# Performance work log

Hardware: AMD Instinct MI355X
Metric: run time of the kernel (lower is better)

The kernel has to match this reference:

```python
import jax, jax.numpy as jnp
import numpy as np

EPS = 1e-5  # torch LayerNorm default


def _ln(x, g, b):
    m = jnp.mean(x, axis=-1, keepdims=True)
    v = jnp.mean((x - m) ** 2, axis=-1, keepdims=True)
    return (x - m) / jnp.sqrt(v + EPS) * g + b


def setup_inputs() -> dict:
    key = jax.random.key(0)
    ks = jax.random.split(key, 16)
    B, C, H, S, FF, BINS = 2048, 20, 256, 64, 512, 128
    f32 = jnp.float32
    def w(k, shape, s=0.02):
        return jax.random.normal(k, shape, f32) * s
    return {
        "bitplanes": jax.random.normal(ks[0], (B, C, 8, 8), f32),
        "conv1_w": w(ks[1], (H, C, 3, 3), 0.05), "conv1_b": jnp.zeros((H,), f32),
        "conv2_w": w(ks[2], (H, H, 3, 3), 0.05), "conv2_b": jnp.zeros((H,), f32),
        "in_proj_w": w(ks[3], (3 * H, H)), "in_proj_b": jnp.zeros((3 * H,), f32),
        "out_proj_w": w(ks[4], (H, H)), "out_proj_b": jnp.zeros((H,), f32),
        "ln1_g": jnp.ones((H,), f32), "ln1_b": jnp.zeros((H,), f32),
        "ff1_w": w(ks[5], (FF, H)), "ff1_b": jnp.zeros((FF,), f32),
        "ff2_w": w(ks[6], (H, FF)), "ff2_b": jnp.zeros((H,), f32),
        "ln2_g": jnp.ones((H,), f32), "ln2_b": jnp.zeros((H,), f32),
        "be1_w": w(ks[7], (H, H * S)), "be1_b": jnp.zeros((H,), f32),
        "be2_w": w(ks[8], (H, H)), "be2_b": jnp.zeros((H,), f32),
        "L1_w": w(ks[9], (H, 3 * H)), "L1_b": jnp.zeros((H,), f32),
        "L2_w": w(ks[10], (H, H)), "L2_b": jnp.zeros((H,), f32),
        "Lln_g": jnp.ones((H,), f32), "Lln_b": jnp.zeros((H,), f32),
        "H1_w": w(ks[11], (H, 2 * H)), "H1_b": jnp.zeros((H,), f32),
        "H2_w": w(ks[12], (H, H)), "H2_b": jnp.zeros((H,), f32),
        "Hln_g": jnp.ones((H,), f32), "Hln_b": jnp.zeros((H,), f32),
        "v1_w": w(ks[13], (H, H)), "v1_b": jnp.zeros((H,), f32),
        "v2_w": w(ks[14], (BINS, H)), "v2_b": jnp.zeros((BINS,), f32),
    }


def reference(bitplanes, conv1_w, conv1_b, conv2_w, conv2_b,
              in_proj_w, in_proj_b, out_proj_w, out_proj_b,
              ln1_g, ln1_b, ff1_w, ff1_b, ff2_w, ff2_b, ln2_g, ln2_b,
              be1_w, be1_b, be2_w, be2_b,
              L1_w, L1_b, L2_w, L2_b, Lln_g, Lln_b,
              H1_w, H1_b, H2_w, H2_b, Hln_g, Hln_b,
              v1_w, v1_b, v2_w, v2_b):
    N, T, Hd, nh = 8, 8, 256, 4
    B = bitplanes.shape[0]
    dn = ('NCHW', 'OIHW', 'NCHW')
    # conv encoder on 8x8 board
    x = jax.nn.relu(jax.lax.conv_general_dilated(bitplanes, conv1_w, (1, 1), 'SAME', dimension_numbers=dn) + conv1_b[None, :, None, None])
    x = jax.nn.relu(jax.lax.conv_general_dilated(x, conv2_w, (1, 1), 'SAME', dimension_numbers=dn) + conv2_b[None, :, None, None])
    x = x.reshape(B, Hd, 64).transpose(0, 2, 1)  # [B, 64, 256]
    # TransformerEncoderLayer (post-norm, eval mode => dropout off)
    qkv = x @ in_proj_w.T + in_proj_b  # [B, 64, 768]
    q, k, v = jnp.split(qkv, 3, axis=-1)
    dh = Hd // nh
    heads = lambda t: t.reshape(B, 64, nh, dh).transpose(0, 2, 1, 3)
    q, k, v = heads(q), heads(k), heads(v)
    scale = 1.0 / float(dh) ** 0.5
    a = jax.nn.softmax(jnp.einsum('bhqd,bhkd->bhqk', q, k) * scale, axis=-1)
    o = jnp.einsum('bhqk,bhkd->bhqd', a, v).transpose(0, 2, 1, 3).reshape(B, 64, Hd)
    o = o @ out_proj_w.T + out_proj_b
    x = _ln(x + o, ln1_g, ln1_b)
    ff = jax.nn.relu(x @ ff1_w.T + ff1_b) @ ff2_w.T + ff2_b
    x = _ln(x + ff, ln2_g, ln2_b)
    xf = x.reshape(B, 64 * Hd)  # [B, 16384]
    be = jax.nn.relu(jax.nn.relu(xf @ be1_w.T + be1_b) @ be2_w.T + be2_b)

    def Lnet(zL, zH):
        h = jax.nn.relu(jnp.concatenate([zL, zH, be], axis=-1) @ L1_w.T + L1_b)
        return _ln(jax.nn.relu(h @ L2_w.T + L2_b), Lln_g, Lln_b)

    def Hnet(zH, zL):
        h = jax.nn.relu(jnp.concatenate([zH, zL], axis=-1) @ H1_w.T + H1_b)
        return _ln(jax.nn.relu(h @ H2_w.T + H2_b), Hln_g, Hln_b)

    z0 = jnp.zeros((B, Hd), x.dtype)

    def step(carry, i):
        zH, zL = carry
        zL = Lnet(zL, zH)
        zH = jnp.where((i + 1) % T == 0, Hnet(zH, zL), zH)  # H update every T steps
        return (zH, zL), None

    (zH, zL), _ = jax.lax.scan(step, (z0, z0), jnp.arange(N * T - 1))
    zL = Lnet(zL, zH)
    zH = Hnet(zH, zL)
    return jax.nn.relu(zH @ v1_w.T + v1_b) @ v2_w.T + v2_b  # [B, 128]
```

## Files before the change

kernel.cpp:

```cpp
#include <hip/hip_runtime.h>
#include <hip/hip_bf16.h>
#include <math.h>

#define DEV __device__ __forceinline__

typedef __attribute__((ext_vector_type(8))) short s16x8;
typedef __attribute__((ext_vector_type(4))) float f32x4;

DEV f32x4 MF(s16x8 a, s16x8 b, f32x4 c) {
    return __builtin_amdgcn_mfma_f32_16x16x32_bf16(a, b, c, 0, 0, 0);
}

DEV void split3(float x, unsigned short& h, unsigned short& m, unsigned short& l) {
    const unsigned u = __float_as_uint(x);
    h = (unsigned short)(u >> 16);
    const float r1 = x - __uint_as_float(u & 0xffff0000u);
    const unsigned u1 = __float_as_uint(r1);
    m = (unsigned short)(u1 >> 16);
    const float r2 = r1 - __uint_as_float(u1 & 0xffff0000u);
    l = (unsigned short)(__float_as_uint(r2) >> 16);
}

DEV void split8store(const float v[8], unsigned short* d) {
    s16x8 vh, vm, vl;
#pragma unroll
    for (int j = 0; j < 8; ++j) {
        unsigned short h, m, l;
        split3(v[j], h, m, l);
        vh[j] = (short)h; vm[j] = (short)m; vl[j] = (short)l;
    }
    *(s16x8*)(d) = vh;
    *(s16x8*)(d + 512) = vm;
    *(s16x8*)(d + 1024) = vl;
}

__global__ void k_tpose(const float* __restrict__ in, float* __restrict__ out, int N, int K) {
    int total = N * K;
    for (int idx = blockIdx.x * blockDim.x + threadIdx.x; idx < total; idx += gridDim.x * blockDim.x) {
        int n = idx / K, k = idx - n * K;
        out[k * N + n] = in[idx];
    }
}

__global__ void k_wpack3(const float* __restrict__ W, unsigned short* __restrict__ WP,
                         int K, int NT, int ldw, int stride, int off) {
    const int idx = blockIdx.x * 256 + threadIdx.x;
    const int total = (K >> 5) * NT * 64;
    if (idx >= total) return;
    const int lane = idx & 63;
    const int nt = (idx >> 6) % NT;
    const int ks = idx / (64 * NT);
    const int col = nt * 16 + (lane & 15);
    const int k0 = ks * 32 + ((lane >> 4) << 3);
    const float* src = W + (size_t)col * ldw + (size_t)k0 * stride + off;
    float v[8];
#pragma unroll
    for (int j = 0; j < 8; ++j) v[j] = src[j * stride];
    split8store(v, WP + (size_t)((ks * NT + nt) * 3) * 512 + lane * 8);
}

__global__ __launch_bounds__(256) void k_conv1(const float* __restrict__ in, const float* __restrict__ w,
                                               const float* __restrict__ bias, float* __restrict__ out) {
    __shared__ __align__(16) float img[20 * 100];
    __shared__ __align__(16) float stg[16 * 260];
    const int b = blockIdx.x;
    const int t = threadIdx.x;
    for (int idx = t; idx < 2000; idx += 256) {
        int c = idx / 100, pp = idx - c * 100;
        int y = pp / 10, x = pp - y * 10;
        float v = 0.f;
        if (y >= 1 && y <= 8 && x >= 1 && x <= 8)
            v = in[((size_t)b * 20 + c) * 64 + (y - 1) * 8 + (x - 1)];
        img[idx] = v;
    }
    __syncthreads();
    const int oc = t;
    float acc[64];
    const float bz = bias[oc];
#pragma unroll
    for (int p = 0; p < 64; ++p) acc[p] = bz;
    const float* wrow = w + oc * 180;
    for (int c = 0; c < 20; ++c) {
#pragma unroll
        for (int k = 0; k < 9; ++k) {
            const int ky = k / 3, kx = k - ky * 3;
            const float wv = wrow[c * 9 + k];
            const int base = c * 100 + ky * 10 + kx;
#pragma unroll
            for (int p = 0; p < 64; ++p)
                acc[p] = fmaf(wv, img[base + p + ((p >> 3) << 1)], acc[p]);
        }
    }
#pragma unroll
    for (int cc = 0; cc < 4; ++cc) {
        __syncthreads();
#pragma unroll
        for (int p = 0; p < 16; ++p) stg[p * 260 + t] = acc[cc * 16 + p];
        __syncthreads();
        for (int idx = t; idx < 4096; idx += 256) {
            const int r = idx >> 8, c = idx & 255;
            out[((size_t)b * 64 + cc * 16 + r) * 256 + c] = fmaxf(stg[r * 260 + c], 0.f);
        }
    }
}

__global__ __launch_bounds__(256) void k_conv2mf(const float* __restrict__ a1,
                                                 const unsigned short* __restrict__ WPC2,
                                                 const float* __restrict__ bias,
                                                 float* __restrict__ xout,
                                                 unsigned short* __restrict__ xh,
                                                 unsigned short* __restrict__ xm,
                                                 unsigned short* __restrict__ xl) {
    __shared__ __align__(16) unsigned short AhS[100 * 132];
    __shared__ __align__(16) unsigned short AmS[100 * 132];
    __shared__ __align__(16) unsigned short AlS[100 * 132];
    const int b = blockIdx.x, t = threadIdx.x;
    const int wv = t >> 6, lane = t & 63;
    f32x4 acc[16];
#pragma unroll
    for (int nt = 0; nt < 16; ++nt) acc[nt] = (f32x4){0.f, 0.f, 0.f, 0.f};
    const int pl = lane & 15;
    const int py = pl >> 3, px = pl & 7;
    const int akoff = (lane >> 4) << 3;
    for (int h = 0; h < 2; ++h) {
        __syncthreads();
        for (int idx = t; idx < 12800; idx += 256) {
            const int pr = idx >> 7, c = idx & 127;
            const int Y = pr / 10, X = pr - Y * 10;
            float v = 0.f;
            if (Y >= 1 && Y <= 8 && X >= 1 && X <= 8)
                v = a1[((size_t)b * 64 + (Y - 1) * 8 + X - 1) * 256 + h * 128 + c];
            unsigned short hh, mm, ll;
            split3(v, hh, mm, ll);
            AhS[pr * 132 + c] = hh;
            AmS[pr * 132 + c] = mm;
            AlS[pr * 132 + c] = ll;
        }
        __syncthreads();
#pragma unroll
        for (int tap = 0; tap < 9; ++tap) {
            const int dy = tap / 3, dx = tap - dy * 3;
            const int prow = (wv * 2 + py + dy) * 10 + px + dx;
            const unsigned short* arh = AhS + prow * 132 + akoff;
            const unsigned short* arm = AmS + prow * 132 + akoff;
            const unsigned short* arl = AlS + prow * 132 + akoff;
#pragma unroll
            for (int ks = 0; ks < 4; ++ks) {
                const s16x8 ah = *(const s16x8*)(arh + ks * 32);
                const s16x8 am = *(const s16x8*)(arm + ks * 32);
                const s16x8 al = *(const s16x8*)(arl + ks * 32);
                const unsigned short* bp = WPC2 + (size_t)(tap * 128 + (h * 4 + ks) * 16) * 1536 + lane * 8;
#pragma unroll
                for (int nt = 0; nt < 16; ++nt) {
                    const unsigned short* bb = bp + nt * 1536;
                    const s16x8 bh = *(const s16x8*)(bb);
                    const s16x8 bm = *(const s16x8*)(bb + 512);
                    const s16x8 bl = *(const s16x8*)(bb + 1024);
                    acc[nt] = MF(ah, bh, acc[nt]);
                    acc[nt] = MF(ah, bm, acc[nt]);
                    acc[nt] = MF(am, bh, acc[nt]);
                    acc[nt] = MF(ah, bl, acc[nt]);
                    acc[nt] = MF(al, bh, acc[nt]);
                    acc[nt] = MF(am, bm, acc[nt]);
                }
            }
        }
    }
    const int prow0 = wv * 16 + ((lane >> 4) << 2);
    const int ccol = lane & 15;
#pragma unroll
    for (int nt = 0; nt < 16; ++nt) {
        const float bz = bias[nt * 16 + ccol];
#pragma unroll
        for (int i = 0; i < 4; ++i) {
            const float v = fmaxf(acc[nt][i] + bz, 0.f);
            const size_t o = ((size_t)b * 64 + prow0 + i) * 256 + nt * 16 + ccol;
            xout[o] = v;
            unsigned short hh, mm, ll;
            split3(v, hh, mm, ll);
            xh[o] = hh;
            xm[o] = mm;
            xl[o] = ll;
        }
    }
}

__global__ __launch_bounds__(512) void k_attn2(const float* __restrict__ qkv,
                                               unsigned short* __restrict__ oh, unsigned short* __restrict__ om,
                                               unsigned short* __restrict__ ol) {
    __shared__ __align__(16) float qs[64 * 65];
    __shared__ __align__(16) float ks[64 * 68];
    __shared__ __align__(16) float vs[64 * 68];
    __shared__ float pmax[8 * 64];
    __shared__ float psum[8 * 64];
    const int b = blockIdx.x, h = blockIdx.y;
    const int t = threadIdx.x;
    for (int idx = t; idx < 1024; idx += 512) {
        const int rr = idx >> 4, cc = (idx & 15) * 4;
        const float* src = qkv + ((size_t)b * 64 + rr) * 768 + h * 64 + cc;
        const float4 q4 = *(const float4*)(src);
        const float4 k4 = *(const float4*)(src + 256);
        const float4 v4 = *(const float4*)(src + 512);
        qs[rr * 65 + cc + 0] = q4.x; qs[rr * 65 + cc + 1] = q4.y;
        qs[rr * 65 + cc + 2] = q4.z; qs[rr * 65 + cc + 3] = q4.w;
        *(float4*)(ks + rr * 68 + cc) = k4;
        *(float4*)(vs + rr * 68 + cc) = v4;
    }
    __syncthreads();
    const int r = t & 63;
    const int cg = t >> 6;
    float sc[8];
#pragma unroll
    for (int j = 0; j < 8; ++j) sc[j] = 0.f;
    for (int kk = 0; kk < 64; kk += 4) {
        float qv[4];
#pragma unroll
        for (int i = 0; i < 4; ++i) qv[i] = qs[r * 65 + kk + i];
#pragma unroll
        for (int j = 0; j < 8; ++j) {
            const float4 kv = *(const float4*)(ks + (cg * 8 + j) * 68 + kk);
            sc[j] = fmaf(qv[0], kv.x, sc[j]); sc[j] = fmaf(qv[1], kv.y, sc[j]);
            sc[j] = fmaf(qv[2], kv.z, sc[j]); sc[j] = fmaf(qv[3], kv.w, sc[j]);
        }
    }
    float pm = -1e30f;
#pragma unroll
    for (int j = 0; j < 8; ++j) { sc[j] *= 0.125f; pm = fmaxf(pm, sc[j]); }
    pmax[cg * 64 + r] = pm;
    __syncthreads();
    float m = pmax[r];
#pragma unroll
    for (int i = 1; i < 8; ++i) m = fmaxf(m, pmax[i * 64 + r]);
    float pe[8], ps = 0.f;
#pragma unroll
    for (int j = 0; j < 8; ++j) { pe[j] = __expf(sc[j] - m); ps += pe[j]; }
    psum[cg * 64 + r] = ps;
    __syncthreads();
    float den = psum[r];
#pragma unroll
    for (int i = 1; i < 8; ++i) den += psum[i * 64 + r];
    const float rden = 1.f / den;
#pragma unroll
    for (int j = 0; j < 8; ++j) qs[r * 65 + cg * 8 + j] = pe[j] * rden;
    __syncthreads();
    float oa[8];
#pragma unroll
    for (int j = 0; j < 8; ++j) oa[j] = 0.f;
    for (int c = 0; c < 64; ++c) {
        const float pv = qs[r * 65 + c];
        const float4 v0 = *(const float4*)(vs + c * 68 + cg * 8);
        const float4 v1 = *(const float4*)(vs + c * 68 + cg * 8 + 4);
        oa[0] = fmaf(pv, v0.x, oa[0]); oa[1] = fmaf(pv, v0.y, oa[1]);
        oa[2] = fmaf(pv, v0.z, oa[2]); oa[3] = fmaf(pv, v0.w, oa[3]);
        oa[4] = fmaf(pv, v1.x, oa[4]); oa[5] = fmaf(pv, v1.y, oa[5]);
        oa[6] = fmaf(pv, v1.z, oa[6]); oa[7] = fmaf(pv, v1.w, oa[7]);
    }
#pragma unroll
    for (int j = 0; j < 8; ++j) ks[r * 68 + cg * 8 + j] = oa[j];
    __syncthreads();
    for (int idx = t; idx < 4096; idx += 512) {
        const int rr = idx >> 6, dd = idx & 63;
        const float v = ks[rr * 68 + dd];
        unsigned short hh, mm, ll;
        split3(v, hh, mm, ll);
        const size_t o = ((size_t)b * 64 + rr) * 256 + h * 64 + dd;
        oh[o] = hh;
        om[o] = mm;
        ol[o] = ll;
    }
}

__global__ __launch_bounds__(256) void k_gemm_mf(
    const unsigned short* __restrict__ Ah, const unsigned short* __restrict__ Am,
    const unsigned short* __restrict__ Al,
    const unsigned short* __restrict__ WP, const float* __restrict__ bias,
    float* __restrict__ Cf, unsigned short* __restrict__ Ch, unsigned short* __restrict__ Cm,
    unsigned short* __restrict__ Cl,
    int M, int N, int K, int kChunk, int relu) {
    const int t = threadIdx.x;
    const int wv = t >> 6, lane = t & 63;
    const int row0 = blockIdx.x * 64 + wv * 16;
    const int col0 = blockIdx.y * 64;
    const int NT = N >> 4;
    const int k0 = blockIdx.z * kChunk;
    const int nks = kChunk >> 5;
    f32x4 acc[4];
#pragma unroll
    for (int nt = 0; nt < 4; ++nt) acc[nt] = (f32x4){0.f, 0.f, 0.f, 0.f};
    const int arow = row0 + (lane & 15);
    const size_t aoff = (size_t)arow * K + k0 + ((lane >> 4) << 3);
    const unsigned short* aph = Ah + aoff;
    const unsigned short* apm = Am + aoff;
    const unsigned short* apl = Al + aoff;
    const unsigned short* bp = WP + ((size_t)((k0 >> 5) * NT + (col0 >> 4))) * 1536 + lane * 8;
    const size_t bstride = (size_t)NT * 1536;
    for (int ks = 0; ks < nks; ++ks) {
        const s16x8 ah = *(const s16x8*)aph;
        const s16x8 am = *(const s16x8*)apm;
        const s16x8 al = *(const s16x8*)apl;
        aph += 32; apm += 32; apl += 32;
#pragma unroll
        for (int nt = 0; nt < 4; ++nt) {
            const unsigned short* bb = bp + nt * 1536;
            const s16x8 bh = *(const s16x8*)(bb);
            const s16x8 bm = *(const s16x8*)(bb + 512);
            const s16x8 bl = *(const s16x8*)(bb + 1024);
            acc[nt] = MF(ah, bh, acc[nt]);
            acc[nt] = MF(ah, bm, acc[nt]);
            acc[nt] = MF(am, bh, acc[nt]);
            acc[nt] = MF(ah, bl, acc[nt]);
            acc[nt] = MF(al, bh, acc[nt]);
            acc[nt] = MF(am, bm, acc[nt]);
        }
        bp += bstride;
    }
    const int crow = row0 + ((lane >> 4) << 2);
    const int ccol = col0 + (lane & 15);
    float bz[4];
#pragma unroll
    for (int nt = 0; nt < 4; ++nt) bz[nt] = bias ? bias[ccol + nt * 16] : 0.f;
    if (Ch) {
#pragma unroll
        for (int nt = 0; nt < 4; ++nt) {
#pragma unroll
            for (int i = 0; i < 4; ++i) {
                float v = acc[nt][i] + bz[nt];
                if (relu) v = fmaxf(v, 0.f);
                unsigned short hh, mm, ll;
                split3(v, hh, mm, ll);
                const size_t o = (size_t)(crow + i) * N + ccol + nt * 16;
                Ch[o] = hh;
                Cm[o] = mm;
                Cl[o] = ll;
            }
        }
    } else {
        float* base = Cf + (size_t)blockIdx.z * M * N;
#pragma unroll
        for (int nt = 0; nt < 4; ++nt) {
#pragma unroll
            for (int i = 0; i < 4; ++i) {
                float v = acc[nt][i] + bz[nt];
                if (relu) v = fmaxf(v, 0.f);
                base[(size_t)(crow + i) * N + ccol + nt * 16] = v;
            }
        }
    }
}

__global__ __launch_bounds__(256) void k_ln_add(float* __restrict__ x, const float* __restrict__ add,
                                                const float* __restrict__ g, const float* __restrict__ bta,
                                                unsigned short* __restrict__ sh, unsigned short* __restrict__ sm,
                                                unsigned short* __restrict__ sl) {
    const int t = threadIdx.x;
    const size_t r = (size_t)blockIdx.x * 4 + (t >> 6);
    const int lane = t & 63;
    float4 xv = *(const float4*)(x + r * 256 + lane * 4);
    const float4 av = *(const float4*)(add + r * 256 + lane * 4);
    const float4 v = make_float4(xv.x + av.x, xv.y + av.y, xv.z + av.z, xv.w + av.w);
    float s = v.x + v.y + v.z + v.w;
    float ss = fmaf(v.x, v.x, fmaf(v.y, v.y, fmaf(v.z, v.z, v.w * v.w)));
#pragma unroll
    for (int m = 32; m; m >>= 1) { s += __shfl_xor(s, m); ss += __shfl_xor(ss, m); }
    const float mean = s * (1.f / 256.f);
    const float var = ss * (1.f / 256.f) - mean * mean;
    const float rstd = rsqrtf(var + 1e-5f);
    const float4 g4 = *(const float4*)(g + lane * 4);
    const float4 b4 = *(const float4*)(bta + lane * 4);
    float4 ov;
    ov.x = (v.x - mean) * rstd * g4.x + b4.x;
    ov.y = (v.y - mean) * rstd * g4.y + b4.y;
    ov.z = (v.z - mean) * rstd * g4.z + b4.z;
    ov.w = (v.w - mean) * rstd * g4.w + b4.w;
    *(float4*)(x + r * 256 + lane * 4) = ov;
    const float vv[4] = {ov.x, ov.y, ov.z, ov.w};
    unsigned short hh[4], mm[4], ll[4];
#pragma unroll
    for (int j = 0; j < 4; ++j) split3(vv[j], hh[j], mm[j], ll[j]);
    *(ushort4*)(sh + r * 256 + lane * 4) = make_ushort4(hh[0], hh[1], hh[2], hh[3]);
    *(ushort4*)(sm + r * 256 + lane * 4) = make_ushort4(mm[0], mm[1], mm[2], mm[3]);
    *(ushort4*)(sl + r * 256 + lane * 4) = make_ushort4(ll[0], ll[1], ll[2], ll[3]);
}

__global__ void k_be1_reduce(const float* __restrict__ parts, const float* __restrict__ bias,
                             unsigned short* __restrict__ oh, unsigned short* __restrict__ om,
                             unsigned short* __restrict__ ol, int n) {
    const int idx = blockIdx.x * blockDim.x + threadIdx.x;
    if (idx < n) {
        float s = bias[idx & 255];
#pragma unroll
        for (int p = 0; p < 8; ++p) s += parts[(size_t)p * n + idx];
        s = fmaxf(s, 0.f);
        unsigned short hh, mm, ll;
        split3(s, hh, mm, ll);
        oh[idx] = hh;
        om[idx] = mm;
        ol[idx] = ll;
    }
}

DEV void splitpass(const float* scr, unsigned short* frag, int t) {
    const int ks = t >> 6, ln = t & 63;
    const int row = ln & 15;
    const int k0 = ks * 32 + ((ln >> 4) << 3);
    const float* s = scr + row * 260 + k0;
    const float4 p = *(const float4*)s;
    const float4 q = *(const float4*)(s + 4);
    const float v[8] = {p.x, p.y, p.z, p.w, q.x, q.y, q.z, q.w};
    split8store(v, frag + (ks * 3) * 512 + ln * 8);
}

DEV void mfma6(f32x4& acc, s16x8 ah, s16x8 am, s16x8 al, const unsigned short* bp) {
    const s16x8 bh = *(const s16x8*)(bp);
    const s16x8 bm = *(const s16x8*)(bp + 512);
    const s16x8 bl = *(const s16x8*)(bp + 1024);
    acc = MF(ah, bh, acc);
    acc = MF(ah, bm, acc);
    acc = MF(am, bh, acc);
    acc = MF(ah, bl, acc);
    acc = MF(al, bh, acc);
    acc = MF(am, bm, acc);
}

DEV void rungemm(f32x4& a0, f32x4& a1, const unsigned short* __restrict__ WP, int KS,
                 const unsigned short* f0, const unsigned short* f1, const unsigned short* f2,
                 int wv, int lane) {
    for (int ks = 0; ks < KS; ++ks) {
        const unsigned short* fa = (ks < 8) ? f0 : ((ks < 16) ? f1 : f2);
        const int kl = ks & 7;
        const unsigned short* ap = fa + (kl * 3) * 512 + lane * 8;
        const s16x8 ah = *(const s16x8*)(ap);
        const s16x8 am = *(const s16x8*)(ap + 512);
        const s16x8 al = *(const s16x8*)(ap + 1024);
        const unsigned short* bp = WP + (size_t)((ks * 16 + wv * 2) * 3) * 512 + lane * 8;
        mfma6(a0, ah, am, al, bp);
        mfma6(a1, ah, am, al, bp + 1536);
    }
}

DEV void storeC(f32x4 a0, f32x4 a1, const float* __restrict__ bias, float* scr, int wv, int lane) {
    const int rb = (lane >> 4) * 4;
    const int c0 = wv * 32 + (lane & 15);
    const float bz0 = bias[c0];
    const float bz1 = bias[c0 + 16];
    scr[(rb + 0) * 260 + c0] = fmaxf(a0[0] + bz0, 0.f);
    scr[(rb + 1) * 260 + c0] = fmaxf(a0[1] + bz0, 0.f);
    scr[(rb + 2) * 260 + c0] = fmaxf(a0[2] + bz0, 0.f);
    scr[(rb + 3) * 260 + c0] = fmaxf(a0[3] + bz0, 0.f);
    scr[(rb + 0) * 260 + c0 + 16] = fmaxf(a1[0] + bz1, 0.f);
    scr[(rb + 1) * 260 + c0 + 16] = fmaxf(a1[1] + bz1, 0.f);
    scr[(rb + 2) * 260 + c0 + 16] = fmaxf(a1[2] + bz1, 0.f);
    scr[(rb + 3) * 260 + c0 + 16] = fmaxf(a1[3] + bz1, 0.f);
}

DEV void lnpass(float* scr, const float* __restrict__ g, const float* __restrict__ bb, int t) {
    const int row = 2 * (t >> 6) + ((t & 63) >> 5);
    const int c0 = (t & 31) * 8;
    float* s = scr + row * 260 + c0;
    const float4 x0 = *(const float4*)s;
    const float4 x1 = *(const float4*)(s + 4);
    float sum = x0.x + x0.y + x0.z + x0.w + x1.x + x1.y + x1.z + x1.w;
    float sq = fmaf(x0.x, x0.x, fmaf(x0.y, x0.y, fmaf(x0.z, x0.z, x0.w * x0.w)));
    sq = fmaf(x1.x, x1.x, fmaf(x1.y, x1.y, fmaf(x1.z, x1.z, fmaf(x1.w, x1.w, sq))));
#pragma unroll
    for (int m = 16; m; m >>= 1) { sum += __shfl_xor(sum, m); sq += __shfl_xor(sq, m); }
    const float mean = sum * (1.f / 256.f);
    const float var = sq * (1.f / 256.f) - mean * mean;
    const float rstd = rsqrtf(var + 1e-5f);
    const float4 g0 = *(const float4*)(g + c0);
    const float4 g1 = *(const float4*)(g + c0 + 4);
    const float4 b0 = *(const float4*)(bb + c0);
    const float4 b1 = *(const float4*)(bb + c0 + 4);
    float4 o0, o1;
    o0.x = (x0.x - mean) * rstd * g0.x + b0.x;
    o0.y = (x0.y - mean) * rstd * g0.y + b0.y;
    o0.z = (x0.z - mean) * rstd * g0.z + b0.z;
    o0.w = (x0.w - mean) * rstd * g0.w + b0.w;
    o1.x = (x1.x - mean) * rstd * g1.x + b1.x;
    o1.y = (x1.y - mean) * rstd * g1.y + b1.y;
    o1.z = (x1.z - mean) * rstd * g1.z + b1.z;
    o1.w = (x1.w - mean) * rstd * g1.w + b1.w;
    *(float4*)s = o0;
    *(float4*)(s + 4) = o1;
}

__global__ __launch_bounds__(512, 1) void k_hrm(const float* __restrict__ be,
        const unsigned short* __restrict__ L1P, const float* __restrict__ L1b,
        const unsigned short* __restrict__ L2P, const float* __restrict__ L2b,
        const float* __restrict__ Lg, const float* __restrict__ Lbt,
        const unsigned short* __restrict__ H1P, const float* __restrict__ H1b,
        const unsigned short* __restrict__ H2P, const float* __restrict__ H2b,
        const float* __restrict__ Hg, const float* __restrict__ Hbt,
        const unsigned short* __restrict__ v1P, const float* __restrict__ v1b,
        const float* __restrict__ v2T, const float* __restrict__ v2b,
        float* __restrict__ out) {
    __shared__ __align__(16) unsigned short fzL[12288];
    __shared__ __align__(16) unsigned short fzH[12288];
    __shared__ __align__(16) unsigned short fbe[12288];
    __shared__ __align__(16) unsigned short fh1[12288];
    __shared__ __align__(16) float scr[16 * 260];
    const int t = threadIdx.x;
    const int b0 = blockIdx.x * 16;
    const int wv = t >> 6, lane = t & 63;
    for (int i = t; i < 12288; i += 512) { fzL[i] = 0; fzH[i] = 0; }
    {
        const int ks = t >> 6, ln = t & 63;
        const int row = ln & 15;
        const int k0 = ks * 32 + ((ln >> 4) << 3);
        const float* s = be + (size_t)(b0 + row) * 256 + k0;
        const float4 p = *(const float4*)s;
        const float4 q = *(const float4*)(s + 4);
        const float v[8] = {p.x, p.y, p.z, p.w, q.x, q.y, q.z, q.w};
        split8store(v, fbe + (ks * 3) * 512 + ln * 8);
    }
    __syncthreads();
    const f32x4 zero4 = {0.f, 0.f, 0.f, 0.f};
    for (int it = 0; it < 64; ++it) {
        f32x4 a0 = zero4, a1 = zero4;
        rungemm(a0, a1, L1P, 24, fzL, fzH, fbe, wv, lane);
        storeC(a0, a1, L1b, scr, wv, lane);
        __syncthreads();
        splitpass(scr, fh1, t);
        __syncthreads();
        a0 = zero4; a1 = zero4;
        rungemm(a0, a1, L2P, 8, fh1, fh1, fh1, wv, lane);
        storeC(a0, a1, L2b, scr, wv, lane);
        __syncthreads();
        lnpass(scr, Lg, Lbt, t);
        __syncthreads();
        splitpass(scr, fzL, t);
        __syncthreads();
        if (((it + 1) & 7) == 0) {
            a0 = zero4; a1 = zero4;
            rungemm(a0, a1, H1P, 16, fzH, fzL, fzL, wv, lane);
            storeC(a0, a1, H1b, scr, wv, lane);
            __syncthreads();
            splitpass(scr, fh1, t);
            __syncthreads();
            a0 = zero4; a1 = zero4;
            rungemm(a0, a1, H2P, 8, fh1, fh1, fh1, wv, lane);
            storeC(a0, a1, H2b, scr, wv, lane);
            __syncthreads();
            lnpass(scr, Hg, Hbt, t);
            __syncthreads();
            splitpass(scr, fzH, t);
            __syncthreads();
        }
    }
    f32x4 a0 = zero4, a1 = zero4;
    rungemm(a0, a1, v1P, 8, fzH, fzH, fzH, wv, lane);
    storeC(a0, a1, v1b, scr, wv, lane);
    __syncthreads();
    for (int idx = t; idx < 2048; idx += 512) {
        const int r = idx >> 7, oo = idx & 127;
        float s = v2b[oo];
        for (int kk = 0; kk < 256; kk += 4) {
            const float4 c4 = *(const float4*)(&scr[r * 260 + kk]);
            s = fmaf(c4.x, v2T[(kk + 0) * 128 + oo], s);
            s = fmaf(c4.y, v2T[(kk + 1) * 128 + oo], s);
            s = fmaf(c4.z, v2T[(kk + 2) * 128 + oo], s);
            s = fmaf(c4.w, v2T[(kk + 3) * 128 + oo], s);
        }
        out[(size_t)(b0 + r) * 128 + oo] = s;
    }
}

extern "C" void kernel_launch(void* const* d_in, const int* in_sizes, int n_in,
                              void* d_out, int out_size, void* d_ws, size_t ws_size,
                              hipStream_t stream) {
    const float* bitplanes  = (const float*)d_in[0];
    const float* conv1_w    = (const float*)d_in[1];
    const float* conv1_b    = (const float*)d_in[2];
    const float* conv2_w    = (const float*)d_in[3];
    const float* conv2_b    = (const float*)d_in[4];
    const float* in_proj_w  = (const float*)d_in[5];
    const float* in_proj_b  = (const float*)d_in[6];
    const float* out_proj_w = (const float*)d_in[7];
    const float* out_proj_b = (const float*)d_in[8];
    const float* ln1_g      = (const float*)d_in[9];
    const float* ln1_b      = (const float*)d_in[10];
    const float* ff1_w      = (const float*)d_in[11];
    const float* ff1_b      = (const float*)d_in[12];
    const float* ff2_w      = (const float*)d_in[13];
    const float* ff2_b      = (const float*)d_in[14];
    const float* ln2_g      = (const float*)d_in[15];
    const float* ln2_b      = (const float*)d_in[16];
    const float* be1_w      = (const float*)d_in[17];
    const float* be1_b      = (const float*)d_in[18];
    const float* be2_w      = (const float*)d_in[19];
    const float* be2_b      = (const float*)d_in[20];
    const float* L1_w       = (const float*)d_in[21];
    const float* L1_b       = (const float*)d_in[22];
    const float* L2_w       = (const float*)d_in[23];
    const float* L2_b       = (const float*)d_in[24];
    const float* Lln_g      = (const float*)d_in[25];
    const float* Lln_b      = (const float*)d_in[26];
    const float* H1_w       = (const float*)d_in[27];
    const float* H1_b       = (const float*)d_in[28];
    const float* H2_w       = (const float*)d_in[29];
    const float* H2_b       = (const float*)d_in[30];
    const float* Hln_g      = (const float*)d_in[31];
    const float* Hln_b      = (const float*)d_in[32];
    const float* v1_w       = (const float*)d_in[33];
    const float* v1_b       = (const float*)d_in[34];
    const float* v2_w       = (const float*)d_in[35];
    const float* v2_b       = (const float*)d_in[36];

    const size_t persist = 9404416ull;
    int CB = 64;
    for (int c = 2048; c >= 64; c >>= 1) {
        size_t needBytes = ((size_t)c * 106880ull + persist) * 4ull;
        if (needBytes <= ws_size) { CB = c; break; }
    }
    const int NCH = 2048 / CB;

    float* ws = (float*)d_ws;
    float* a1buf = ws;
    float* xbuf  = a1buf + (size_t)CB * 16384;
    float* sbuf  = xbuf + (size_t)CB * 16384;
    float* tbuf  = sbuf + (size_t)CB * 24576;
    float* bemf  = tbuf + (size_t)CB * 49152;
    float* wpQf  = bemf + (size_t)CB * 384;
    float* v2T   = wpQf + 294912;
    float* L1Pf  = v2T + 32768;
    float* L2Pf  = L1Pf + 294912;
    float* H1Pf  = L2Pf + 98304;
    float* H2Pf  = H1Pf + 196608;
    float* v1Pf  = H2Pf + 98304;
    float* beB   = v1Pf + 98304;
    float* wpOf  = beB + 524288;
    float* wpF1f = wpOf + 98304;
    float* wpF2f = wpF1f + 196608;
    float* wpB1f = wpF2f + 196608;
    float* wpB2f = wpB1f + 6291456;
    float* wpC2f = wpB2f + 98304;

    unsigned short* soh = (unsigned short*)sbuf;
    unsigned short* som = soh + (size_t)CB * 16384;
    unsigned short* sol = som + (size_t)CB * 16384;
    unsigned short* tbh = (unsigned short*)tbuf;
    unsigned short* tbm = tbh + (size_t)CB * 32768;
    unsigned short* tbl = tbm + (size_t)CB * 32768;
    unsigned short* bemh = (unsigned short*)bemf;
    unsigned short* bemm = bemh + (size_t)CB * 256;
    unsigned short* beml = bemm + (size_t)CB * 256;
    unsigned short* wpQ = (unsigned short*)wpQf;
    unsigned short* L1P = (unsigned short*)L1Pf;
    unsigned short* L2P = (unsigned short*)L2Pf;
    unsigned short* H1P = (unsigned short*)H1Pf;
    unsigned short* H2P = (unsigned short*)H2Pf;
    unsigned short* v1P = (unsigned short*)v1Pf;
    unsigned short* wpO = (unsigned short*)wpOf;
    unsigned short* wpF1 = (unsigned short*)wpF1f;
    unsigned short* wpF2 = (unsigned short*)wpF2f;
    unsigned short* wpB1 = (unsigned short*)wpB1f;
    unsigned short* wpB2 = (unsigned short*)wpB2f;
    unsigned short* wpC2 = (unsigned short*)wpC2f;

    k_tpose<<<64, 256, 0, stream>>>(v2_w, v2T, 128, 256);
    k_wpack3<<<96, 256, 0, stream>>>(in_proj_w, wpQ, 256, 48, 256, 1, 0);
    k_wpack3<<<96, 256, 0, stream>>>(L1_w, L1P, 768, 16, 768, 1, 0);
    k_wpack3<<<32, 256, 0, stream>>>(L2_w, L2P, 256, 16, 256, 1, 0);
    k_wpack3<<<64, 256, 0, stream>>>(H1_w, H1P, 512, 16, 512, 1, 0);
    k_wpack3<<<32, 256, 0, stream>>>(H2_w, H2P, 256, 16, 256, 1, 0);
    k_wpack3<<<32, 256, 0, stream>>>(v1_w, v1P, 256, 16, 256, 1, 0);
    k_wpack3<<<32, 256, 0, stream>>>(out_proj_w, wpO, 256, 16, 256, 1, 0);
    k_wpack3<<<64, 256, 0, stream>>>(ff1_w, wpF1, 256, 32, 256, 1, 0);
    k_wpack3<<<64, 256, 0, stream>>>(ff2_w, wpF2, 512, 16, 512, 1, 0);
    k_wpack3<<<2048, 256, 0, stream>>>(be1_w, wpB1, 16384, 16, 16384, 1, 0);
    k_wpack3<<<32, 256, 0, stream>>>(be2_w, wpB2, 256, 16, 256, 1, 0);
    for (int tap = 0; tap < 9; ++tap)
        k_wpack3<<<32, 256, 0, stream>>>(conv2_w, wpC2 + (size_t)tap * 196608, 256, 16, 2304, 9, tap);

    for (int ch = 0; ch < NCH; ++ch) {
        const float* bp_c = bitplanes + (size_t)ch * CB * 20 * 64;
        k_conv1<<<CB, 256, 0, stream>>>(bp_c, conv1_w, conv1_b, a1buf);
        k_conv2mf<<<CB, 256, 0, stream>>>(a1buf, wpC2, conv2_b, xbuf, soh, som, sol);
        k_gemm_mf<<<dim3(CB, 12, 1), 256, 0, stream>>>(soh, som, sol, wpQ, in_proj_b,
                                                       tbuf, nullptr, nullptr, nullptr,
                                                       CB * 64, 768, 256, 256, 0);
        k_attn2<<<dim3(CB, 4), 512, 0, stream>>>(tbuf, soh, som, sol);
        k_gemm_mf<<<dim3(CB, 4, 1), 256, 0, stream>>>(soh, som, sol, wpO, out_proj_b,
                                                      a1buf, nullptr, nullptr, nullptr,
                                                      CB * 64, 256, 256, 256, 0);
        k_ln_add<<<CB * 16, 256, 0, stream>>>(xbuf, a1buf, ln1_g, ln1_b, soh, som, sol);
        k_gemm_mf<<<dim3(CB, 8, 1), 256, 0, stream>>>(soh, som, sol, wpF1, ff1_b,
                                                      nullptr, tbh, tbm, tbl,
                                                      CB * 64, 512, 256, 256, 1);
        k_gemm_mf<<<dim3(CB, 4, 1), 256, 0, stream>>>(tbh, tbm, tbl, wpF2, ff2_b,
                                                      a1buf, nullptr, nullptr, nullptr,
                                                      CB * 64, 256, 512, 512, 0);
        k_ln_add<<<CB * 16, 256, 0, stream>>>(xbuf, a1buf, ln2_g, ln2_b, soh, som, sol);
        k_gemm_mf<<<dim3(CB / 64, 4, 8), 256, 0, stream>>>(soh, som, sol, wpB1, nullptr,
                                                           tbuf, nullptr, nullptr, nullptr,
                                                           CB, 256, 16384, 2048, 0);
        k_be1_reduce<<<CB, 256, 0, stream>>>(tbuf, be1_b, bemh, bemm, beml, CB * 256);
        k_gemm_mf<<<dim3(CB / 64, 4, 1), 256, 0, stream>>>(bemh, bemm, beml, wpB2, be2_b,
                                                           beB + (size_t)ch * CB * 256, nullptr, nullptr, nullptr,
                                                           CB, 256, 256, 256, 1);
    }

    k_hrm<<<128, 512, 0, stream>>>(beB, L1P, L1_b, L2P, L2_b, Lln_g, Lln_b,
                                   H1P, H1_b, H2P, H2_b, Hln_g, Hln_b,
                                   v1P, v1_b, v2T, v2_b, (float*)d_out);
}
```

Before: 5.361 ms.

## Fuse QKV projection into attention kernel and add 128-row MFMA GEMM

Replaces the separate QKV GEMM plus attention kernel with one kernel per board that computes Q/K/V for each head via split-bf16 MFMA directly into shared memory, then runs softmax attention. This removes the fp32 QKV intermediate write and read through global memory. Also adds a GEMM variant where each wave computes two 16-row tiles, so weight fragments are reused across 128 rows per block, and uses it for out_proj, ff1 and ff2. The fused kernel serialises the four heads in one block and rereads A fragments from global memory, which may lower parallelism.

```diff
diff --git a/kernel.cpp b/kernel.cpp
--- a/kernel.cpp
+++ b/kernel.cpp
@@ -32,6 +32,18 @@
     *(s16x8*)(d) = vh;
     *(s16x8*)(d + 512) = vm;
     *(s16x8*)(d + 1024) = vl;
+}
+
+DEV void mfma6(f32x4& acc, s16x8 ah, s16x8 am, s16x8 al, const unsigned short* bp) {
+    const s16x8 bh = *(const s16x8*)(bp);
+    const s16x8 bm = *(const s16x8*)(bp + 512);
+    const s16x8 bl = *(const s16x8*)(bp + 1024);
+    acc = MF(ah, bh, acc);
+    acc = MF(ah, bm, acc);
+    acc = MF(am, bh, acc);
+    acc = MF(ah, bl, acc);
+    acc = MF(al, bh, acc);
+    acc = MF(am, bm, acc);
 }
 
 __global__ void k_tpose(const float* __restrict__ in, float* __restrict__ out, int N, int K) {
@@ -152,16 +164,7 @@
                 const unsigned short* bp = WPC2 + (size_t)(tap * 128 + (h * 4 + ks) * 16) * 1536 + lane * 8;
 #pragma unroll
                 for (int nt = 0; nt < 16; ++nt) {
-                    const unsigned short* bb = bp + nt * 1536;
-                    const s16x8 bh = *(const s16x8*)(bb);
-                    const s16x8 bm = *(const s16x8*)(bb + 512);
-                    const s16x8 bl = *(const s16x8*)(bb + 1024);
-                    acc[nt] = MF(ah, bh, acc[nt]);
-                    acc[nt] = MF(ah, bm, acc[nt]);
-                    acc[nt] = MF(am, bh, acc[nt]);
-                    acc[nt] = MF(ah, bl, acc[nt]);
-                    acc[nt] = MF(al, bh, acc[nt]);
-                    acc[nt] = MF(am, bm, acc[nt]);
+                    mfma6(acc[nt], ah, am, al, bp + nt * 1536);
                 }
             }
         }
@@ -185,88 +188,126 @@
     }
 }
 
-__global__ __launch_bounds__(512) void k_attn2(const float* __restrict__ qkv,
-                                               unsigned short* __restrict__ oh, unsigned short* __restrict__ om,
-                                               unsigned short* __restrict__ ol) {
+__global__ __launch_bounds__(512) void k_attn3(
+    const unsigned short* __restrict__ Ah, const unsigned short* __restrict__ Am,
+    const unsigned short* __restrict__ Al,
+    const unsigned short* __restrict__ wpQ, const float* __restrict__ bqkv,
+    unsigned short* __restrict__ oh, unsigned short* __restrict__ om,
+    unsigned short* __restrict__ ol) {
     __shared__ __align__(16) float qs[64 * 65];
-    __shared__ __align__(16) float ks[64 * 68];
-    __shared__ __align__(16) float vs[64 * 68];
+    __shared__ __align__(16) float kss[64 * 68];
+    __shared__ __align__(16) float vss[64 * 68];
     __shared__ float pmax[8 * 64];
     __shared__ float psum[8 * 64];
-    const int b = blockIdx.x, h = blockIdx.y;
+    const int b = blockIdx.x;
     const int t = threadIdx.x;
-    for (int idx = t; idx < 1024; idx += 512) {
-        const int rr = idx >> 4, cc = (idx & 15) * 4;
-        const float* src = qkv + ((size_t)b * 64 + rr) * 768 + h * 64 + cc;
-        const float4 q4 = *(const float4*)(src);
-        const float4 k4 = *(const float4*)(src + 256);
-        const float4 v4 = *(const float4*)(src + 512);
-        qs[rr * 65 + cc + 0] = q4.x; qs[rr * 65 + cc + 1] = q4.y;
-        qs[rr * 65 + cc + 2] = q4.z; qs[rr * 65 + cc + 3] = q4.w;
-        *(float4*)(ks + rr * 68 + cc) = k4;
-        *(float4*)(vs + rr * 68 + cc) = v4;
-    }
-    __syncthreads();
-    const int r = t & 63;
-    const int cg = t >> 6;
-    float sc[8];
-#pragma unroll
-    for (int j = 0; j < 8; ++j) sc[j] = 0.f;
-    for (int kk = 0; kk < 64; kk += 4) {
-        float qv[4];
-#pragma unroll
-        for (int i = 0; i < 4; ++i) qv[i] = qs[r * 65 + kk + i];
-#pragma unroll
-        for (int j = 0; j < 8; ++j) {
-            const float4 kv = *(const float4*)(ks + (cg * 8 + j) * 68 + kk);
-            sc[j] = fmaf(qv[0], kv.x, sc[j]); sc[j] = fmaf(qv[1], kv.y, sc[j]);
-            sc[j] = fmaf(qv[2], kv.z, sc[j]); sc[j] = fmaf(qv[3], kv.w, sc[j]);
-        }
-    }
-    float pm = -1e30f;
-#pragma unroll
-    for (int j = 0; j < 8; ++j) { sc[j] *= 0.125f; pm = fmaxf(pm, sc[j]); }
-    pmax[cg * 64 + r] = pm;
-    __syncthreads();
-    float m = pmax[r];
-#pragma unroll
-    for (int i = 1; i < 8; ++i) m = fmaxf(m, pmax[i * 64 + r]);
-    float pe[8], ps = 0.f;
-#pragma unroll
-    for (int j = 0; j < 8; ++j) { pe[j] = __expf(sc[j] - m); ps += pe[j]; }
-    psum[cg * 64 + r] = ps;
-    __syncthreads();
-    float den = psum[r];
-#pragma unroll
-    for (int i = 1; i < 8; ++i) den += psum[i * 64 + r];
-    const float rden = 1.f / den;
-#pragma unroll
-    for (int j = 0; j < 8; ++j) qs[r * 65 + cg * 8 + j] = pe[j] * rden;
-    __syncthreads();
-    float oa[8];
-#pragma unroll
-    for (int j = 0; j < 8; ++j) oa[j] = 0.f;
-    for (int c = 0; c < 64; ++c) {
-        const float pv = qs[r * 65 + c];
-        const float4 v0 = *(const float4*)(vs + c * 68 + cg * 8);
-        const float4 v1 = *(const float4*)(vs + c * 68 + cg * 8 + 4);
-        oa[0] = fmaf(pv, v0.x, oa[0]); oa[1] = fmaf(pv, v0.y, oa[1]);
-        oa[2] = fmaf(pv, v0.z, oa[2]); oa[3] = fmaf(pv, v0.w, oa[3]);
-        oa[4] = fmaf(pv, v1.x, oa[4]); oa[5] = fmaf(pv, v1.y, oa[5]);
-        oa[6] = fmaf(pv, v1.z, oa[6]); oa[7] = fmaf(pv, v1.w, oa[7]);
-    }
-#pragma unroll
-    for (int j = 0; j < 8; ++j) ks[r * 68 + cg * 8 + j] = oa[j];
-    __syncthreads();
-    for (int idx = t; idx < 4096; idx += 512) {
-        const int rr = idx >> 6, dd = idx & 63;
-        const float v = ks[rr * 68 + dd];
-        unsigned short hh, mm, ll;
-        split3(v, hh, mm, ll);
-        const size_t o = ((size_t)b * 64 + rr) * 256 + h * 64 + dd;
-        oh[o] = hh;
-        om[o] = mm;
-        ol[o] = ll;
+    const int wv = t >> 6, lane = t & 63;
+    const f32x4 zero4 = {0.f, 0.f, 0.f, 0.f};
+    for (int h = 0; h < 4; ++h) {
+        f32x4 acc[6];
+#pragma unroll
+        for (int e = 0; e < 6; ++e) acc[e] = zero4;
+#pragma unroll
+        for (int e = 0; e < 6; ++e) {
+            const int p = wv * 6 + e;
+            const int m = p >> 4;
+            const int idx = p & 15;
+            const int tile = idx >> 2;
+            const int ntl = idx & 3;
+            const int ntg = m * 16 + h * 4 + ntl;
+            const int arow = b * 64 + tile * 16 + (lane & 15);
+            const size_t aoff = (size_t)arow * 256 + ((lane >> 4) << 3);
+            const unsigned short* aph = Ah + aoff;
+            const unsigned short* apm = Am + aoff;
+            const unsigned short* apl = Al + aoff;
+            const unsigned short* bp = wpQ + (size_t)ntg * 1536 + lane * 8;
+#pragma unroll
+            for (int ks = 0; ks < 8; ++ks) {
+                const s16x8 ah = *(const s16x8*)(aph + ks * 32);
+                const s16x8 am = *(const s16x8*)(apm + ks * 32);
+                const s16x8 al = *(const s16x8*)(apl + ks * 32);
+                mfma6(acc[e], ah, am, al, bp + (size_t)ks * 73728);
+            }
+        }
+        __syncthreads();
+#pragma unroll
+        for (int e = 0; e < 6; ++e) {
+            const int p = wv * 6 + e;
+            const int m = p >> 4;
+            const int idx = p & 15;
+            const int tile = idx >> 2;
+            const int ntl = idx & 3;
+            const int colL = ntl * 16 + (lane & 15);
+            const float bz = bqkv[m * 256 + h * 64 + colL];
+            const int rb = tile * 16 + ((lane >> 4) << 2);
+            float* dst = (m == 0) ? qs : ((m == 1) ? kss : vss);
+            const int strd = (m == 0) ? 65 : 68;
+#pragma unroll
+            for (int i = 0; i < 4; ++i)
+                dst[(rb + i) * strd + colL] = acc[e][i] + bz;
+        }
+        __syncthreads();
+        const int r = t & 63;
+        const int cg = t >> 6;
+        float sc[8];
+#pragma unroll
+        for (int j = 0; j < 8; ++j) sc[j] = 0.f;
+        for (int kk = 0; kk < 64; kk += 4) {
+            float qv[4];
+#pragma unroll
+            for (int i = 0; i < 4; ++i) qv[i] = qs[r * 65 + kk + i];
+#pragma unroll
+            for (int j = 0; j < 8; ++j) {
+                const float4 kv = *(const float4*)(kss + (cg * 8 + j) * 68 + kk);
+                sc[j] = fmaf(qv[0], kv.x, sc[j]); sc[j] = fmaf(qv[1], kv.y, sc[j]);
+                sc[j] = fmaf(qv[2], kv.z, sc[j]); sc[j] = fmaf(qv[3], kv.w, sc[j]);
+            }
+        }
+        float pm = -1e30f;
+#pragma unroll
+        for (int j = 0; j < 8; ++j) { sc[j] *= 0.125f; pm = fmaxf(pm, sc[j]); }
+        pmax[cg * 64 + r] = pm;
+        __syncthreads();
+        float m = pmax[r];
+#pragma unroll
+        for (int i = 1; i < 8; ++i) m = fmaxf(m, pmax[i * 64 + r]);
+        float pe[8], ps = 0.f;
+#pragma unroll
+        for (int j = 0; j < 8; ++j) { pe[j] = __expf(sc[j] - m); ps += pe[j]; }
+        psum[cg * 64 + r] = ps;
+        __syncthreads();
+        float den = psum[r];
+#pragma unroll
+        for (int i = 1; i < 8; ++i) den += psum[i * 64 + r];
+        const float rden = 1.f / den;
+#pragma unroll
+        for (int j = 0; j < 8; ++j) qs[r * 65 + cg * 8 + j] = pe[j] * rden;
+        __syncthreads();
+        float oa[8];
+#pragma unroll
+        for (int j = 0; j < 8; ++j) oa[j] = 0.f;
+        for (int c = 0; c < 64; ++c) {
+            const float pv = qs[r * 65 + c];
+            const float4 v0 = *(const float4*)(vss + c * 68 + cg * 8);
+            const float4 v1 = *(const float4*)(vss + c * 68 + cg * 8 + 4);
+            oa[0] = fmaf(pv, v0.x, oa[0]); oa[1] = fmaf(pv, v0.y, oa[1]);
+            oa[2] = fmaf(pv, v0.z, oa[2]); oa[3] = fmaf(pv, v0.w, oa[3]);
+            oa[4] = fmaf(pv, v1.x, oa[4]); oa[5] = fmaf(pv, v1.y, oa[5]);
+            oa[6] = fmaf(pv, v1.z, oa[6]); oa[7] = fmaf(pv, v1.w, oa[7]);
+        }
+#pragma unroll
+        for (int j = 0; j < 8; ++j) kss[r * 68 + cg * 8 + j] = oa[j];
+        __syncthreads();
+        for (int idx = t; idx < 4096; idx += 512) {
+            const int rr = idx >> 6, dd = idx & 63;
+            const float v = kss[rr * 68 + dd];
+            unsigned short hh, mm, ll;
+            split3(v, hh, mm, ll);
+            const size_t o = ((size_t)b * 64 + rr) * 256 + h * 64 + dd;
+            oh[o] = hh;
+            om[o] = mm;
+            ol[o] = ll;
+        }
     }
 }
 
@@ -301,16 +342,7 @@
         aph += 32; apm += 32; apl += 32;
 #pragma unroll
         for (int nt = 0; nt < 4; ++nt) {
-            const unsigned short* bb = bp + nt * 1536;
-            const s16x8 bh = *(const s16x8*)(bb);
-            const s16x8 bm = *(const s16x8*)(bb + 512);
-            const s16x8 bl = *(const s16x8*)(bb + 1024);
-            acc[nt] = MF(ah, bh, acc[nt]);
-            acc[nt] = MF(ah, bm, acc[nt]);
-            acc[nt] = MF(am, bh, acc[nt]);
-            acc[nt] = MF(ah, bl, acc[nt]);
-            acc[nt] = MF(al, bh, acc[nt]);
-            acc[nt] = MF(am, bm, acc[nt]);
+            mfma6(acc[nt], ah, am, al, bp + nt * 1536);
         }
         bp += bstride;
     }
@@ -343,6 +375,96 @@
                 float v = acc[nt][i] + bz[nt];
                 if (relu) v = fmaxf(v, 0.f);
                 base[(size_t)(crow + i) * N + ccol + nt * 16] = v;
+            }
+        }
+    }
+}
+
+__global__ __launch_bounds__(256) void k_gemm_mf128(
+    const unsigned short* __restrict__ Ah, const unsigned short* __restrict__ Am,
+    const unsigned short* __restrict__ Al,
+    const unsigned short* __restrict__ WP, const float* __restrict__ bias,
+    float* __restrict__ Cf, unsigned short* __restrict__ Ch, unsigned short* __restrict__ Cm,
+    unsigned short* __restrict__ Cl,
+    int M, int N, int K, int relu) {
+    const int t = threadIdx.x;
+    const int wv = t >> 6, lane = t & 63;
+    const int row0 = blockIdx.x * 128 + wv * 32;
+    const int col0 = blockIdx.y * 64;
+    const int NT = N >> 4;
+    const int nks = K >> 5;
+    f32x4 acc0[4], acc1[4];
+#pragma unroll
+    for (int nt = 0; nt < 4; ++nt) {
+        acc0[nt] = (f32x4){0.f, 0.f, 0.f, 0.f};
+        acc1[nt] = (f32x4){0.f, 0.f, 0.f, 0.f};
+    }
+    const size_t aoff0 = (size_t)(row0 + (lane & 15)) * K + ((lane >> 4) << 3);
+    const size_t aoff1 = aoff0 + (size_t)16 * K;
+    const unsigned short* bp = WP + (size_t)(col0 >> 4) * 1536 + lane * 8;
+    const size_t bstride = (size_t)NT * 1536;
+    for (int ks = 0; ks < nks; ++ks) {
+        const size_t ao = ks * 32;
+        const s16x8 a0h = *(const s16x8*)(Ah + aoff0 + ao);
+        const s16x8 a0m = *(const s16x8*)(Am + aoff0 + ao);
+        const s16x8 a0l = *(const s16x8*)(Al + aoff0 + ao);
+        const s16x8 a1h = *(const s16x8*)(Ah + aoff1 + ao);
+        const s16x8 a1m = *(const s16x8*)(Am + aoff1 + ao);
+        const s16x8 a1l = *(const s16x8*)(Al + aoff1 + ao);
+#pragma unroll
+        for (int nt = 0; nt < 4; ++nt) {
+            const unsigned short* bb = bp + nt * 1536;
+            const s16x8 bh = *(const s16x8*)(bb);
+            const s16x8 bm = *(const s16x8*)(bb + 512);
+            const s16x8 bl = *(const s16x8*)(bb + 1024);
+            acc0[nt] = MF(a0h, bh, acc0[nt]);
+            acc0[nt] = MF(a0h, bm, acc0[nt]);
+            acc0[nt] = MF(a0m, bh, acc0[nt]);
+            acc0[nt] = MF(a0h, bl, acc0[nt]);
+            acc0[nt] = MF(a0l, bh, acc0[nt]);
+            acc0[nt] = MF(a0m, bm, acc0[nt]);
+            acc1[nt] = MF(a1h, bh, acc1[nt]);
+            acc1[nt] = MF(a1h, bm, acc1[nt]);
+            acc1[nt] = MF(a1m, bh, acc1[nt]);
+            acc1[nt] = MF(a1h, bl, acc1[nt]);
+            acc1[nt] = MF(a1l, bh, acc1[nt]);
+            acc1[nt] = MF(a1m, bm, acc1[nt]);
+        }
+        bp += bstride;
+    }
+    const int crow0 = row0 + ((lane >> 4) << 2);
+    const int ccol = col0 + (lane & 15);
+    float bz[4];
+#pragma unroll
+    for (int nt = 0; nt < 4; ++nt) bz[nt] = bias ? bias[ccol + nt * 16] : 0.f;
+#pragma unroll
+    for (int half = 0; half < 2; ++half) {
+        const int crow = crow0 + half * 16;
+        f32x4* ac = half ? acc1 : acc0;
+        if (Ch) {
+#pragma unroll
+            for (int nt = 0; nt < 4; ++nt) {
+#pragma unroll
+                for (int i = 0; i < 4; ++i) {
+                    float v = ac[nt][i] + bz[nt];
+                    if (relu) v = fmaxf(v, 0.f);
+                    unsigned short hh, mm, ll;
+                    split3(v, hh, mm, ll);
+                    const size_t o = (size_t)(crow + i) * N + ccol + nt * 16;
+                    Ch[o] = hh;
+                    Cm[o] = mm;
+                    Cl[o] = ll;
+                }
+            }
+        } else {
+#pragma unroll
+            for (int nt = 0; nt < 4; ++nt) {
+#pragma unroll
+                for (int i = 0; i < 4; ++i) {
+                    float v = ac[nt][i] + bz[nt];
+                    if (relu) v = fmaxf(v, 0.f);
+                    Cf[(size_t)(crow + i) * N + ccol + nt * 16] = v;
+                }
             }
         }
     }
@@ -408,18 +530,6 @@
     const float4 q = *(const float4*)(s + 4);
     const float v[8] = {p.x, p.y, p.z, p.w, q.x, q.y, q.z, q.w};
     split8store(v, frag + (ks * 3) * 512 + ln * 8);
-}
-
-DEV void mfma6(f32x4& acc, s16x8 ah, s16x8 am, s16x8 al, const unsigned short* bp) {
-    const s16x8 bh = *(const s16x8*)(bp);
-    const s16x8 bm = *(const s16x8*)(bp + 512);
-    const s16x8 bl = *(const s16x8*)(bp + 1024);
-    acc = MF(ah, bh, acc);
-    acc = MF(ah, bm, acc);
-    acc = MF(am, bh, acc);
-    acc = MF(ah, bl, acc);
-    acc = MF(al, bh, acc);
-    acc = MF(am, bm, acc);
 }
 
 DEV void rungemm(f32x4& a0, f32x4& a1, const unsigned short* __restrict__ WP, int KS,
@@ -641,6 +751,9 @@
     unsigned short* tbh = (unsigned short*)tbuf;
     unsigned short* tbm = tbh + (size_t)CB * 32768;
     unsigned short* tbl = tbm + (size_t)CB * 32768;
+    unsigned short* obh = (unsigned short*)tbuf;
+    unsigned short* obm = obh + (size_t)CB * 16384;
+    unsigned short* obl = obm + (size_t)CB * 16384;
     unsigned short* bemh = (unsigned short*)bemf;
     unsigned short* bemm = bemh + (size_t)CB * 256;
     unsigned short* beml = bemm + (size_t)CB * 256;
@@ -676,20 +789,17 @@
         const float* bp_c = bitplanes + (size_t)ch * CB * 20 * 64;
         k_conv1<<<CB, 256, 0, stream>>>(bp_c, conv1_w, conv1_b, a1buf);
         k_conv2mf<<<CB, 256, 0, stream>>>(a1buf, wpC2, conv2_b, xbuf, soh, som, sol);
-        k_gemm_mf<<<dim3(CB, 12, 1), 256, 0, stream>>>(soh, som, sol, wpQ, in_proj_b,
-                                                       tbuf, nullptr, nullptr, nullptr,
-                                                       CB * 64, 768, 256, 256, 0);
-        k_attn2<<<dim3(CB, 4), 512, 0, stream>>>(tbuf, soh, som, sol);
-        k_gemm_mf<<<dim3(CB, 4, 1), 256, 0, stream>>>(soh, som, sol, wpO, out_proj_b,
-                                                      a1buf, nullptr, nullptr, nullptr,
-                                                      CB * 64, 256, 256, 256, 0);
+        k_attn3<<<CB, 512, 0, stream>>>(soh, som, sol, wpQ, in_proj_b, obh, obm, obl);
+        k_gemm_mf128<<<dim3(CB / 2, 4), 256, 0, stream>>>(obh, obm, obl, wpO, out_proj_b,
+                                                          a1buf, nullptr, nullptr, nullptr,
+                                                          CB * 64, 256, 256, 0);
         k_ln_add<<<CB * 16, 256, 0, stream>>>(xbuf, a1buf, ln1_g, ln1_b, soh, som, sol);
-        k_gemm_mf<<<dim3(CB, 8, 1), 256, 0, stream>>>(soh, som, sol, wpF1, ff1_b,
-                                                      nullptr, tbh, tbm, tbl,
-                                                      CB * 64, 512, 256, 256, 1);
-        k_gemm_mf<<<dim3(CB, 4, 1), 256, 0, stream>>>(tbh, tbm, tbl, wpF2, ff2_b,
-                                                      a1buf, nullptr, nullptr, nullptr,
-                                                      CB * 64, 256, 512, 512, 0);
+        k_gemm_mf128<<<dim3(CB / 2, 8), 256, 0, stream>>>(soh, som, sol, wpF1, ff1_b,
+                                                          nullptr, tbh, tbm, tbl,
+                                                          CB * 64, 512, 256, 1);
+        k_gemm_mf128<<<dim3(CB / 2, 4), 256, 0, stream>>>(tbh, tbm, tbl, wpF2, ff2_b,
+                                                          a1buf, nullptr, nullptr, nullptr,
+                                                          CB * 64, 256, 512, 0);
         k_ln_add<<<CB * 16, 256, 0, stream>>>(xbuf, a1buf, ln2_g, ln2_b, soh, som, sol);
         k_gemm_mf<<<dim3(CB / 64, 4, 8), 256, 0, stream>>>(soh, som, sol, wpB1, nullptr,
                                                            tbuf, nullptr, nullptr, nullptr,
```

New measurement: 7.069 ms. 1.32x slower.
